# Kernel optimization log

Measured on AMD Instinct MI355X. Metric: run time of the kernel, lower is better.

Reference implementation:

```python
import jax, jax.numpy as jnp
import numpy as np
import math

NUM_HEADS = 16
NUM_KV_HEADS = 4
HEAD_DIM = 128
HIDDEN = 2048
ROPE_BASE = 10000.0


def setup_inputs() -> dict:
    key = jax.random.key(0)
    ks = jax.random.split(key, 6)
    B, S = 1, 4096
    hidden_states = jax.random.normal(ks[0], (B, S, HIDDEN), dtype=jnp.float32)
    attention_mask = jnp.ones((B, S), dtype=jnp.int32)
    position_ids = jnp.broadcast_to(jnp.arange(S, dtype=jnp.int32)[None, :], (B, S))
    sc = 1.0 / math.sqrt(HIDDEN)
    wq = jax.random.normal(ks[1], (HIDDEN, NUM_HEADS * HEAD_DIM), dtype=jnp.float32) * sc
    wk = jax.random.normal(ks[2], (HIDDEN, NUM_KV_HEADS * HEAD_DIM), dtype=jnp.float32) * sc
    wv = jax.random.normal(ks[3], (HIDDEN, NUM_KV_HEADS * HEAD_DIM), dtype=jnp.float32) * sc
    wo = jax.random.normal(ks[4], (NUM_HEADS * HEAD_DIM, HIDDEN), dtype=jnp.float32) * sc
    return {"hidden_states": hidden_states, "attention_mask": attention_mask,
            "position_ids": position_ids, "wq": wq, "wk": wk, "wv": wv, "wo": wo}


def _rotate_half(x):
    x1, x2 = jnp.split(x, 2, axis=-1)
    return jnp.concatenate((-x2, x1), axis=-1)


def _rope_tables(seq_len, dtype):
    inv_freq = 1.0 / (ROPE_BASE ** (jnp.arange(0, HEAD_DIM, 2, dtype=jnp.float32) / HEAD_DIM))
    t = jnp.arange(seq_len, dtype=jnp.float32)
    freqs = jnp.outer(t, inv_freq)                       # [S, hd/2]
    emb = jnp.concatenate((freqs, freqs), axis=-1)       # [S, hd]
    return jnp.cos(emb).astype(dtype), jnp.sin(emb).astype(dtype)


def reference(hidden_states, attention_mask, position_ids, wq, wk, wv, wo):
    B, S, _ = hidden_states.shape
    dtype = hidden_states.dtype
    # projections -> [B, H, S, hd]
    q = (hidden_states @ wq).reshape(B, S, NUM_HEADS, HEAD_DIM).transpose(0, 2, 1, 3)
    k = (hidden_states @ wk).reshape(B, S, NUM_KV_HEADS, HEAD_DIM).transpose(0, 2, 1, 3)
    v = (hidden_states @ wv).reshape(B, S, NUM_KV_HEADS, HEAD_DIM).transpose(0, 2, 1, 3)
    # RoPE
    cos_t, sin_t = _rope_tables(S, dtype)
    cos = cos_t[position_ids][:, None]                   # [B,1,S,hd]
    sin = sin_t[position_ids][:, None]
    q = q * cos + _rotate_half(q) * sin
    k = k * cos + _rotate_half(k) * sin
    # GQA repeat
    n_rep = NUM_HEADS // NUM_KV_HEADS
    k = jnp.repeat(k, n_rep, axis=1)
    v = jnp.repeat(v, n_rep, axis=1)
    # scores + causal mask + padding mask
    scores = jnp.einsum('bhqd,bhkd->bhqk', q, k) / math.sqrt(HEAD_DIM)
    neg = jnp.finfo(scores.dtype).min
    causal = jnp.triu(jnp.full((S, S), neg, dtype=scores.dtype), k=1)
    scores = scores + causal[None, None]
    pad = (1.0 - attention_mask.astype(scores.dtype))[:, None, None, :] * neg
    scores = scores + pad
    attn = jax.nn.softmax(scores.astype(jnp.float32), axis=-1).astype(dtype)
    out = jnp.einsum('bhqk,bhkd->bhqd', attn, v)
    out = out.transpose(0, 2, 1, 3).reshape(B, S, NUM_HEADS * HEAD_DIM)
    return out @ wo
```

## Files before the change

### kernel.cpp

```cpp
#include <hip/hip_runtime.h>
#include <cstdint>
#include <cstddef>

typedef unsigned short ushort_t;
typedef short    bf16x8 __attribute__((ext_vector_type(8)));
typedef float    f32x4  __attribute__((ext_vector_type(4)));
typedef uint4    __attribute__((may_alias)) uint4_a;
typedef ushort4  __attribute__((may_alias)) ushort4_a;
typedef float4   __attribute__((may_alias)) float4_a;
typedef float2   __attribute__((may_alias)) float2_a;
typedef unsigned __attribute__((may_alias)) uint_a;

constexpr int SEQ = 4096, HID = 2048, NHEADS = 16, NKVH = 4, HDIM = 128;
constexpr int QD  = NHEADS * HDIM;
constexpr int KVD = NKVH * HDIM;
constexpr int KVL = 2 * KVD;
constexpr int NPART = 56;

static __device__ __forceinline__ float bf2f(ushort_t u) {
    return __uint_as_float(((unsigned)u) << 16);
}
static __device__ __forceinline__ ushort_t f2bf(float f) {
    unsigned x = __float_as_uint(f);
    unsigned r = x + 0x7FFFu + ((x >> 16) & 1u);
    return (ushort_t)(r >> 16);
}
static __device__ __forceinline__ unsigned pack2(float lo, float hi) {
    return (unsigned)f2bf(lo) | ((unsigned)f2bf(hi) << 16);
}
static __device__ __forceinline__ unsigned cvt_pk(float lo, float hi) {
    unsigned r;
    asm("v_cvt_pk_bf16_f32 %0, %1, %2" : "=v"(r) : "v"(lo), "v"(hi));
    return r;
}

static __device__ __forceinline__ void gld16(const ushort_t* g, ushort_t* l) {
    __builtin_amdgcn_global_load_lds(
        (const __attribute__((address_space(1))) unsigned*)g,
        (__attribute__((address_space(3))) unsigned*)l, 16, 0, 0);
}

__global__ __launch_bounds__(256) void cast_f32_bf16(
    const float* __restrict__ in, ushort_t* __restrict__ out, int n)
{
    int i = (blockIdx.x * 256 + threadIdx.x) * 8;
    if (i >= n) return;
    float4 a = *(const float4_a*)(in + i);
    float4 b = *(const float4_a*)(in + i + 4);
    uint4 o;
    o.x = pack2(a.x, a.y); o.y = pack2(a.z, a.w);
    o.z = pack2(b.x, b.y); o.w = pack2(b.z, b.w);
    *(uint4_a*)(out + i) = o;
}

__global__ __launch_bounds__(256) void transpose_cast(
    const float* __restrict__ W, ushort_t* __restrict__ WT, int K, int N)
{
    __shared__ float tl[32][36];
    const int k0 = blockIdx.x * 32, n0 = blockIdx.y * 32;
    const int t  = threadIdx.x;
    {
        int i = t >> 3, jb = (t & 7) * 4;
        *(float4_a*)&tl[i][jb] = *(const float4_a*)(W + (size_t)(k0 + i) * N + n0 + jb);
    }
    __syncthreads();
    {
        int n = t >> 3, kb = (t & 7) * 4;
        ushort4 o;
        o.x = f2bf(tl[kb + 0][n]); o.y = f2bf(tl[kb + 1][n]);
        o.z = f2bf(tl[kb + 2][n]); o.w = f2bf(tl[kb + 3][n]);
        *(ushort4_a*)(WT + (size_t)(n0 + n) * K + k0 + kb) = o;
    }
}

__global__ __launch_bounds__(256) void gemm_mfma(
    const ushort_t* __restrict__ A, int lda,
    const ushort_t* __restrict__ Bt, int ldb,
    void* __restrict__ C1, int ld1, void* __restrict__ C2, int ld2,
    int split, int N, int K, int out_f32)
{
    __shared__ ushort_t as[128 * 32];
    __shared__ ushort_t bs[128 * 32];

    const int t    = threadIdx.x;
    const int mb   = blockIdx.y * 128, nb = blockIdx.x * 128;
    const int w    = t >> 6, lane = t & 63, quad = lane >> 4, l15 = lane & 15;
    const int wm   = (w >> 1) * 64, wn = (w & 1) * 64;

    const int dr_row = lane >> 2, dr_c = lane & 3;
    const int rA0 = w * 16 + dr_row, rA1 = 64 + w * 16 + dr_row;
    const ushort_t* a0p = A  + (size_t)(mb + rA0) * lda + (dr_c ^ (rA0 & 3)) * 8;
    const ushort_t* a1p = A  + (size_t)(mb + rA1) * lda + (dr_c ^ (rA1 & 3)) * 8;
    const ushort_t* b0p = Bt + (size_t)(nb + rA0) * ldb + (dr_c ^ (rA0 & 3)) * 8;
    const ushort_t* b1p = Bt + (size_t)(nb + rA1) * ldb + (dr_c ^ (rA1 & 3)) * 8;
    ushort_t* asb0 = &as[(w) * 512];        ushort_t* asb1 = &as[(4 + w) * 512];
    ushort_t* bsb0 = &bs[(w) * 512];        ushort_t* bsb1 = &bs[(4 + w) * 512];

    f32x4 acc[4][4];
#pragma unroll
    for (int i = 0; i < 4; i++)
#pragma unroll
        for (int j = 0; j < 4; j++) acc[i][j] = (f32x4)0.f;

    const int chunk = quad ^ (l15 & 3);

    for (int kb = 0; kb < K; kb += 32) {
        __syncthreads();
        gld16(a0p + kb, asb0);
        gld16(a1p + kb, asb1);
        gld16(b0p + kb, bsb0);
        gld16(b1p + kb, bsb1);
        __syncthreads();

        bf16x8 af[4], bf[4];
#pragma unroll
        for (int mt = 0; mt < 4; mt++)
            af[mt] = *(const bf16x8*)&as[(wm + mt * 16 + l15) * 32 + chunk * 8];
#pragma unroll
        for (int nt = 0; nt < 4; nt++)
            bf[nt] = *(const bf16x8*)&bs[(wn + nt * 16 + l15) * 32 + chunk * 8];
#pragma unroll
        for (int mt = 0; mt < 4; mt++)
#pragma unroll
            for (int nt = 0; nt < 4; nt++)
                acc[mt][nt] = __builtin_amdgcn_mfma_f32_16x16x32_bf16(
                    af[mt], bf[nt], acc[mt][nt], 0, 0, 0);
    }

#pragma unroll
    for (int mt = 0; mt < 4; mt++)
#pragma unroll
        for (int nt = 0; nt < 4; nt++) {
            int colg = nb + wn + nt * 16 + l15;
#pragma unroll
            for (int r = 0; r < 4; r++) {
                int row = mb + wm + mt * 16 + quad * 4 + r;
                float v = acc[mt][nt][r];
                if (out_f32)            ((float*)C1)[(size_t)row * ld1 + colg] = v;
                else if (colg < split)  ((ushort_t*)C1)[(size_t)row * ld1 + colg] = f2bf(v);
                else                    ((ushort_t*)C2)[(size_t)row * ld2 + colg - split] = f2bf(v);
            }
        }
}

__global__ __launch_bounds__(256) void rope_both(
    ushort_t* __restrict__ qb, ushort_t* __restrict__ kvb,
    const int* __restrict__ pos_ids)
{
    int idx  = blockIdx.x * 256 + threadIdx.x;
    int i    = idx & 63;
    int rem  = idx >> 6;
    int hs   = rem % (NHEADS + NKVH);
    int s    = rem / (NHEADS + NKVH);
    if (s >= SEQ) return;

    float pos = (float)pos_ids[s];
    float ang = pos * __expf(-(float)i * 0.14391156831212787f);
    float c, sn;
    sincosf(ang, &sn, &c);

    ushort_t* p = (hs < NHEADS)
        ? qb  + (size_t)s * QD  + hs * HDIM
        : kvb + (size_t)s * KVL + (hs - NHEADS) * HDIM;
    float x0 = bf2f(p[i]);
    float x1 = bf2f(p[i + 64]);
    p[i]      = f2bf(x0 * c - x1 * sn);
    p[i + 64] = f2bf(x1 * c + x0 * sn);
}

__global__ __launch_bounds__(512, 4) void flash_mfma(
    const ushort_t* Q, const ushort_t* __restrict__ KV,
    const int* __restrict__ amask, ushort_t* O,
    ushort_t* __restrict__ Opart, float2* __restrict__ ML)
{
    __shared__ ushort_t ks[64][136];
    __shared__ ushort_t vt[128][72];
    __shared__ float    bias[64];

    const int t = threadIdx.x, w = t >> 6, lane = t & 63;
    const int quad = lane >> 4, l15 = lane & 15;
    const int h = blockIdx.x, kvh = h >> 2;
    const int s = blockIdx.y;
    const int kcol = kvh * HDIM, vcol = KVD + kvh * HDIM;
    const float scale2 = 0.08838834764831845f * 1.44269504088896340f;

    int tile, ktb, kte, pid;
    bool multi;
    if (s < 8)       { tile = 15 - s;        ktb = 0; kte = 2 * tile + 2; multi = false; pid = 0; }
    else if (s < 64) {
        int cs = s - 8;
        int c;
        if (cs < 24) { tile = 16 + cs / 3; c = cs - (tile - 16) * 3; }
        else         { int d = cs - 24; tile = 24 + (d >> 2); c = d & 3; }
        int nkt = 2 * tile + 2;
        ktb = c * 16; kte = (ktb + 16 < nkt) ? ktb + 16 : nkt;
        multi = true; pid = h * NPART + cs;
    }
    else             { tile = 7 - (s - 64);  ktb = 0; kte = 2 * tile + 2; multi = false; pid = 0; }

    const int q0  = tile * 128;
    const int q0w = q0 + w * 16;

    const int krow = t >> 3,  kdo = (t & 7) * 16;
    const int vkp  = t & 31,  vdg = t >> 5;

    int bpi[4];
#pragma unroll
    for (int t4 = 0; t4 < 4; t4++)
        bpi[t4] = ((2 * (quad & 1) + (t4 >> 1)) * 16 + l15) * 4;
    const bool hi_half = (quad >> 1) != 0;

    bf16x8 qf[4];
    {
        const ushort_t* qp = Q + (size_t)(q0w + l15) * QD + h * HDIM;
#pragma unroll
        for (int c = 0; c < 4; c++)
            qf[c] = *(const bf16x8*)(qp + c * 32 + quad * 8);
    }

    f32x4 accO[8];
#pragma unroll
    for (int j = 0; j < 8; j++) accO[j] = (f32x4)0.f;
    float m_s = -1e30f, l_s = 0.f;

    uint4 kst[2], va, vb;
    float bst = 0.f;
    auto stage_load = [&](int kt) {
        const int k0 = kt * 64;
        const ushort_t* kp = KV + (size_t)(k0 + krow) * KVL + kcol + kdo;
        kst[0] = *(const uint4_a*)kp;
        kst[1] = *(const uint4_a*)(kp + 8);
        const ushort_t* vp = KV + (size_t)(k0 + 2 * vkp) * KVL + vcol + vdg * 8;
        va = *(const uint4_a*)vp;
        vb = *(const uint4_a*)(vp + KVL);
        if (t < 64) bst = amask[k0 + t] ? 0.f : -1e30f;
    };

    stage_load(ktb);

    for (int kt = ktb; kt < kte; kt++) {
        const int k0 = kt * 64;
        __syncthreads();
        *(uint4_a*)&ks[krow][kdo]     = kst[0];
        *(uint4_a*)&ks[krow][kdo + 8] = kst[1];
        {
            unsigned aw[4] = {va.x, va.y, va.z, va.w};
            unsigned bw[4] = {vb.x, vb.y, vb.z, vb.w};
#pragma unroll
            for (int i = 0; i < 4; i++) {
                *(uint_a*)&vt[vdg * 8 + 2 * i][2 * vkp] =
                    (aw[i] & 0xFFFFu) | (bw[i] << 16);
                *(uint_a*)&vt[vdg * 8 + 2 * i + 1][2 * vkp] =
                    (aw[i] >> 16) | (bw[i] & 0xFFFF0000u);
            }
        }
        if (t < 64) bias[t] = bst;
        __syncthreads();
        if (kt + 1 < kte) stage_load(kt + 1);

        if (k0 > q0w + 15) continue;

        f32x4 sx[4];
#pragma unroll
        for (int mt = 0; mt < 4; mt++) sx[mt] = (f32x4)0.f;
        __builtin_amdgcn_s_setprio(1);
#pragma unroll
        for (int c = 0; c < 4; c++)
#pragma unroll
            for (int mt = 0; mt < 4; mt++) {
                bf16x8 kf = *(const bf16x8*)&ks[mt * 16 + l15][c * 32 + quad * 8];
                sx[mt] = __builtin_amdgcn_mfma_f32_16x16x32_bf16(kf, qf[c], sx[mt], 0, 0, 0);
            }
        __builtin_amdgcn_s_setprio(0);

        const int qg = q0w + l15;
        const bool full = (k0 + 63 <= q0w);
        float p[4][4];
        float mx = -1e30f;
#pragma unroll
        for (int mt = 0; mt < 4; mt++) {
            float4 b4 = *(const float4_a*)&bias[mt * 16 + quad * 4];
            float br[4] = {b4.x, b4.y, b4.z, b4.w};
#pragma unroll
            for (int r = 0; r < 4; r++) {
                float v = fmaf(sx[mt][r], scale2, br[r]);
                if (!full) {
                    int kg = k0 + mt * 16 + quad * 4 + r;
                    v = (kg > qg) ? -1e30f : v;
                }
                p[mt][r] = v;
                mx = fmaxf(mx, v);
            }
        }
        mx = fmaxf(mx, __shfl_xor(mx, 16));
        mx = fmaxf(mx, __shfl_xor(mx, 32));
        const bool renorm = !__all(mx <= m_s + 8.f);
        const float mnew = renorm ? fmaxf(m_s, mx) : m_s;
        float sum = 0.f;
        unsigned wlo[4], whi[4];
#pragma unroll
        for (int mt = 0; mt < 4; mt++) {
            float p0 = exp2f(p[mt][0] - mnew);
            float p1 = exp2f(p[mt][1] - mnew);
            float p2 = exp2f(p[mt][2] - mnew);
            float p3 = exp2f(p[mt][3] - mnew);
            sum += (p0 + p1) + (p2 + p3);
            wlo[mt] = cvt_pk(p0, p1);
            whi[mt] = cvt_pk(p2, p3);
        }
        sum += __shfl_xor(sum, 16);
        sum += __shfl_xor(sum, 32);

        if (renorm) {
            float alpha = exp2f(m_s - mnew);
            l_s *= alpha;
            float a0 = __shfl(alpha, quad * 4 + 0);
            float a1 = __shfl(alpha, quad * 4 + 1);
            float a2 = __shfl(alpha, quad * 4 + 2);
            float a3 = __shfl(alpha, quad * 4 + 3);
#pragma unroll
            for (int j = 0; j < 8; j++) {
                f32x4 a = accO[j];
                a[0] *= a0; a[1] *= a1; a[2] *= a2; a[3] *= a3;
                accO[j] = a;
            }
        }
        m_s = mnew;
        l_s += sum;

#pragma unroll
        for (int kc = 0; kc < 2; kc++) {
            union { unsigned u[4]; bf16x8 v; } pf;
#pragma unroll
            for (int t4 = 0; t4 < 4; t4++) {
                unsigned slo = (t4 & 1) ? whi[2 * kc]     : wlo[2 * kc];
                unsigned shi = (t4 & 1) ? whi[2 * kc + 1] : wlo[2 * kc + 1];
                int ra = __builtin_amdgcn_ds_bpermute(bpi[t4], (int)slo);
                int rb = __builtin_amdgcn_ds_bpermute(bpi[t4], (int)shi);
                pf.u[t4] = (unsigned)(hi_half ? rb : ra);
            }
            __builtin_amdgcn_s_setprio(1);
#pragma unroll
            for (int n8 = 0; n8 < 8; n8++) {
                bf16x8 vf = *(const bf16x8*)&vt[n8 * 16 + l15][kc * 32 + quad * 8];
                accO[n8] = __builtin_amdgcn_mfma_f32_16x16x32_bf16(pf.v, vf, accO[n8], 0, 0, 0);
            }
            __builtin_amdgcn_s_setprio(0);
        }
    }

    if (!multi) {
        float linv = 1.0f / l_s;
#pragma unroll
        for (int r = 0; r < 4; r++) {
            float lr = __shfl(linv, quad * 4 + r);
            int row = q0w + quad * 4 + r;
            ushort_t* op = O + (size_t)row * QD + h * HDIM;
#pragma unroll
            for (int n8 = 0; n8 < 8; n8++)
                op[n8 * 16 + l15] = f2bf(accO[n8][r] * lr);
        }
    } else {
        ushort_t* op = Opart + (size_t)pid * (128 * 128);
#pragma unroll
        for (int r = 0; r < 4; r++) {
            int row = w * 16 + quad * 4 + r;
#pragma unroll
            for (int n8 = 0; n8 < 8; n8++)
                op[row * 128 + n8 * 16 + l15] = f2bf(accO[n8][r]);
        }
        if (quad == 0)
            ML[pid * 128 + w * 16 + l15] = make_float2(m_s, l_s);
    }
}

__global__ __launch_bounds__(256) void combine_partials(
    const ushort_t* __restrict__ P, const float2* __restrict__ ML,
    ushort_t* __restrict__ O)
{
    __shared__ float wc[4][128];
    const int h = blockIdx.x >> 4, tt = blockIdx.x & 15, tile = 16 + tt;
    const int nc = (tile < 24) ? 3 : 4;
    const int pid0 = h * NPART + ((tile < 24) ? tt * 3 : 24 + (tile - 24) * 4);
    const int tid = threadIdx.x;

    if (tid < 128) {
        const int row = tid;
        float m_[4], l_[4];
        float M = -1e30f;
#pragma unroll
        for (int c = 0; c < 4; c++) {
            if (c < nc) {
                float2 v = *(const float2_a*)&ML[(pid0 + c) * 128 + row];
                m_[c] = v.x; l_[c] = v.y; M = fmaxf(M, v.x);
            } else { m_[c] = -1e30f; l_[c] = 0.f; }
        }
        float L = 0.f, wgt[4];
#pragma unroll
        for (int c = 0; c < 4; c++) { wgt[c] = exp2f(m_[c] - M); L += wgt[c] * l_[c]; }
        const float inv = 1.0f / L;
#pragma unroll
        for (int c = 0; c < 4; c++) wc[c][row] = (c < nc) ? wgt[c] * inv : 0.f;
    }
    __syncthreads();

#pragma unroll
    for (int p = 0; p < 4; p++) {
        const int idx = p * 256 + tid;
        const int row = idx >> 3, seg = idx & 7;
        const size_t pb = (size_t)row * 128 + seg * 16;
        float acc[16];
#pragma unroll
        for (int j = 0; j < 16; j++) acc[j] = 0.f;
#pragma unroll
        for (int c = 0; c < 4; c++) {
            if (c < nc) {
                const ushort_t* pp = P + (size_t)(pid0 + c) * (128 * 128) + pb;
                uint4 v0 = *(const uint4_a*)pp;
                uint4 v1 = *(const uint4_a*)(pp + 8);
                const float wv_ = wc[c][row];
                unsigned u[8] = {v0.x, v0.y, v0.z, v0.w, v1.x, v1.y, v1.z, v1.w};
#pragma unroll
                for (int j = 0; j < 8; j++) {
                    acc[2 * j]     += wv_ * bf2f((ushort_t)(u[j] & 0xFFFFu));
                    acc[2 * j + 1] += wv_ * bf2f((ushort_t)(u[j] >> 16));
                }
            }
        }
        ushort_t* op = O + (size_t)(tile * 128 + row) * QD + h * HDIM + seg * 16;
        uint4 o0, o1;
        o0.x = pack2(acc[0],  acc[1]);  o0.y = pack2(acc[2],  acc[3]);
        o0.z = pack2(acc[4],  acc[5]);  o0.w = pack2(acc[6],  acc[7]);
        o1.x = pack2(acc[8],  acc[9]);  o1.y = pack2(acc[10], acc[11]);
        o1.z = pack2(acc[12], acc[13]); o1.w = pack2(acc[14], acc[15]);
        *(uint4_a*)op       = o0;
        *(uint4_a*)(op + 8) = o1;
    }
}

extern "C" void kernel_launch(void* const* d_in, const int* in_sizes, int n_in,
                              void* d_out, int out_size, void* d_ws, size_t ws_size,
                              hipStream_t stream)
{
    const float* x     = (const float*)d_in[0];
    const int*   amask = (const int*)d_in[1];
    const int*   pos   = (const int*)d_in[2];
    const float* wq    = (const float*)d_in[3];
    const float* wk    = (const float*)d_in[4];
    const float* wv    = (const float*)d_in[5];
    const float* wo    = (const float*)d_in[6];
    float* out = (float*)d_out;

    ushort_t* wqkvT = (ushort_t*)d_out;
    ushort_t* xb    = wqkvT + (size_t)3072 * HID;

    ushort_t* qbuf  = (ushort_t*)d_ws;
    ushort_t* kvbuf = qbuf + (size_t)SEQ * QD;
    ushort_t* woT   = kvbuf;

    ushort_t* opart = (ushort_t*)d_out;
    float2*   mlbuf = (float2*)((char*)d_out + (size_t)16 * NPART * 128 * 128 * 2);

    cast_f32_bf16<<<SEQ * HID / 8 / 256, 256, 0, stream>>>(x, xb, SEQ * HID);
    transpose_cast<<<dim3(HID / 32, QD / 32),  256, 0, stream>>>(wq, wqkvT, HID, QD);
    transpose_cast<<<dim3(HID / 32, KVD / 32), 256, 0, stream>>>(wk, wqkvT + (size_t)QD * HID, HID, KVD);
    transpose_cast<<<dim3(HID / 32, KVD / 32), 256, 0, stream>>>(wv, wqkvT + (size_t)(QD + KVD) * HID, HID, KVD);

    gemm_mfma<<<dim3(3072 / 128, SEQ / 128), 256, 0, stream>>>(
        xb, HID, wqkvT, HID, qbuf, QD, kvbuf, KVL, QD, 3072, HID, 0);

    rope_both<<<SEQ * (NHEADS + NKVH) * 64 / 256, 256, 0, stream>>>(qbuf, kvbuf, pos);

    flash_mfma<<<dim3(NHEADS, 72), 512, 0, stream>>>(
        qbuf, kvbuf, amask, qbuf, opart, mlbuf);
    combine_partials<<<dim3(256), 256, 0, stream>>>(opart, mlbuf, qbuf);

    transpose_cast<<<dim3(QD / 32, HID / 32), 256, 0, stream>>>(wo, woT, QD, HID);
    gemm_mfma<<<dim3(HID / 128, SEQ / 128), 256, 0, stream>>>(
        qbuf, QD, woT, QD, out, HID, out, HID, HID, HID, QD, 1);
}
```

Baseline: 449.2 us.

## Double-buffer flash attention K/V tiles with async LDS loads and swizzle

The flash attention kernel now keeps two LDS buffers for K, V^T and the mask bias. The next K tile is fetched with direct global-to-LDS loads (gld16) into an XOR-swizzled unpadded layout, and the next V tile is loaded into registers and stored after compute. This cuts the per-iteration barriers from two to one and overlaps loads with the MFMA work. The three QKV weight transpose launches are also merged into one kernel. The cost is doubled LDS use, which may limit occupancy under launch_bounds(512,4).

```diff
diff --git a/kernel.cpp b/kernel.cpp
--- a/kernel.cpp
+++ b/kernel.cpp
@@ -73,6 +73,31 @@
     }
 }
 
+__global__ __launch_bounds__(256) void transpose_cast_qkv(
+    const float* __restrict__ wq, const float* __restrict__ wk,
+    const float* __restrict__ wv, ushort_t* __restrict__ WT)
+{
+    __shared__ float tl[32][36];
+    const int k0 = blockIdx.x * 32, nb = blockIdx.y * 32;
+    const int t  = threadIdx.x;
+    const float* W; int n0, N;
+    if (nb < 2048)      { W = wq; n0 = nb;        N = QD;  }
+    else if (nb < 2560) { W = wk; n0 = nb - 2048; N = KVD; }
+    else                { W = wv; n0 = nb - 2560; N = KVD; }
+    {
+        int i = t >> 3, jb = (t & 7) * 4;
+        *(float4_a*)&tl[i][jb] = *(const float4_a*)(W + (size_t)(k0 + i) * N + n0 + jb);
+    }
+    __syncthreads();
+    {
+        int n = t >> 3, kb = (t & 7) * 4;
+        ushort4 o;
+        o.x = f2bf(tl[kb + 0][n]); o.y = f2bf(tl[kb + 1][n]);
+        o.z = f2bf(tl[kb + 2][n]); o.w = f2bf(tl[kb + 3][n]);
+        *(ushort4_a*)(WT + (size_t)(nb + n) * HID + k0 + kb) = o;
+    }
+}
+
 __global__ __launch_bounds__(256) void gemm_mfma(
     const ushort_t* __restrict__ A, int lda,
     const ushort_t* __restrict__ Bt, int ldb,
@@ -173,9 +198,9 @@
     const int* __restrict__ amask, ushort_t* O,
     ushort_t* __restrict__ Opart, float2* __restrict__ ML)
 {
-    __shared__ ushort_t ks[64][136];
-    __shared__ ushort_t vt[128][72];
-    __shared__ float    bias[64];
+    __shared__ ushort_t ks[2][64 * 128];
+    __shared__ ushort_t vt[2][128 * 72];
+    __shared__ float    bias[2][64];
 
     const int t = threadIdx.x, w = t >> 6, lane = t & 63;
     const int quad = lane >> 4, l15 = lane & 15;
@@ -201,7 +226,8 @@
     const int q0  = tile * 128;
     const int q0w = q0 + w * 16;
 
-    const int krow = t >> 3,  kdo = (t & 7) * 16;
+    const int kRow = w * 4 + quad;
+    const int klc  = l15 ^ (kRow & 7);
     const int vkp  = t & 31,  vdg = t >> 5;
 
     int bpi[4];
@@ -210,6 +236,11 @@
         bpi[t4] = ((2 * (quad & 1) + (t4 >> 1)) * 16 + l15) * 4;
     const bool hi_half = (quad >> 1) != 0;
 
+    int pco[4];
+#pragma unroll
+    for (int c = 0; c < 4; c++)
+        pco[c] = ((4 * c + quad) ^ (l15 & 7)) * 8;
+
     bf16x8 qf[4];
     {
         const ushort_t* qp = Q + (size_t)(q0w + l15) * QD + h * HDIM;
@@ -223,130 +254,138 @@
     for (int j = 0; j < 8; j++) accO[j] = (f32x4)0.f;
     float m_s = -1e30f, l_s = 0.f;
 
-    uint4 kst[2], va, vb;
+    uint4 va, vb;
     float bst = 0.f;
-    auto stage_load = [&](int kt) {
-        const int k0 = kt * 64;
-        const ushort_t* kp = KV + (size_t)(k0 + krow) * KVL + kcol + kdo;
-        kst[0] = *(const uint4_a*)kp;
-        kst[1] = *(const uint4_a*)(kp + 8);
-        const ushort_t* vp = KV + (size_t)(k0 + 2 * vkp) * KVL + vcol + vdg * 8;
+    auto stage_k = [&](int kt, int b) {
+        const ushort_t* g0 = KV + (size_t)(kt * 64 + kRow) * KVL + kcol + klc * 8;
+        gld16(g0, &ks[b][w * 512]);
+        gld16(g0 + (size_t)32 * KVL, &ks[b][4096 + w * 512]);
+    };
+    auto vload = [&](int kt) {
+        const ushort_t* vp = KV + (size_t)(kt * 64 + 2 * vkp) * KVL + vcol + vdg * 8;
         va = *(const uint4_a*)vp;
         vb = *(const uint4_a*)(vp + KVL);
-        if (t < 64) bst = amask[k0 + t] ? 0.f : -1e30f;
+        bst = (t < 64) ? (amask[kt * 64 + t] ? 0.f : -1e30f) : 0.f;
     };
-
-    stage_load(ktb);
+    auto vstore = [&](int b) {
+        unsigned aw[4] = {va.x, va.y, va.z, va.w};
+        unsigned bw[4] = {vb.x, vb.y, vb.z, vb.w};
+#pragma unroll
+        for (int i = 0; i < 4; i++) {
+            *(uint_a*)&vt[b][(vdg * 8 + 2 * i) * 72 + 2 * vkp] =
+                (aw[i] & 0xFFFFu) | (bw[i] << 16);
+            *(uint_a*)&vt[b][(vdg * 8 + 2 * i + 1) * 72 + 2 * vkp] =
+                (aw[i] >> 16) | (bw[i] & 0xFFFF0000u);
+        }
+        if (t < 64) bias[b][t] = bst;
+    };
+
+    stage_k(ktb, 0);
+    vload(ktb);
+    vstore(0);
+    __syncthreads();
 
     for (int kt = ktb; kt < kte; kt++) {
+        const int cur = (kt - ktb) & 1;
         const int k0 = kt * 64;
+        const bool more = (kt + 1 < kte);
+        if (more) {
+            stage_k(kt + 1, cur ^ 1);
+            vload(kt + 1);
+        }
+
+        if (k0 <= q0w + 15) {
+            f32x4 sx[4];
+#pragma unroll
+            for (int mt = 0; mt < 4; mt++) sx[mt] = (f32x4)0.f;
+            __builtin_amdgcn_s_setprio(1);
+#pragma unroll
+            for (int c = 0; c < 4; c++)
+#pragma unroll
+                for (int mt = 0; mt < 4; mt++) {
+                    bf16x8 kf = *(const bf16x8*)&ks[cur][(mt * 16 + l15) * 128 + pco[c]];
+                    sx[mt] = __builtin_amdgcn_mfma_f32_16x16x32_bf16(kf, qf[c], sx[mt], 0, 0, 0);
+                }
+            __builtin_amdgcn_s_setprio(0);
+
+            const int qg = q0w + l15;
+            const bool full = (k0 + 63 <= q0w);
+            float p[4][4];
+            float mx = -1e30f;
+#pragma unroll
+            for (int mt = 0; mt < 4; mt++) {
+                float4 b4 = *(const float4_a*)&bias[cur][mt * 16 + quad * 4];
+                float br[4] = {b4.x, b4.y, b4.z, b4.w};
+#pragma unroll
+                for (int r = 0; r < 4; r++) {
+                    float v = fmaf(sx[mt][r], scale2, br[r]);
+                    if (!full) {
+                        int kg = k0 + mt * 16 + quad * 4 + r;
+                        v = (kg > qg) ? -1e30f : v;
+                    }
+                    p[mt][r] = v;
+                    mx = fmaxf(mx, v);
+                }
+            }
+            mx = fmaxf(mx, __shfl_xor(mx, 16));
+            mx = fmaxf(mx, __shfl_xor(mx, 32));
+            const bool renorm = !__all(mx <= m_s + 8.f);
+            const float mnew = renorm ? fmaxf(m_s, mx) : m_s;
+            float sum = 0.f;
+            unsigned wlo[4], whi[4];
+#pragma unroll
+            for (int mt = 0; mt < 4; mt++) {
+                float p0 = exp2f(p[mt][0] - mnew);
+                float p1 = exp2f(p[mt][1] - mnew);
+                float p2 = exp2f(p[mt][2] - mnew);
+                float p3 = exp2f(p[mt][3] - mnew);
+                sum += (p0 + p1) + (p2 + p3);
+                wlo[mt] = cvt_pk(p0, p1);
+                whi[mt] = cvt_pk(p2, p3);
+            }
+            sum += __shfl_xor(sum, 16);
+            sum += __shfl_xor(sum, 32);
+
+            if (renorm) {
+                float alpha = exp2f(m_s - mnew);
+                l_s *= alpha;
+                float a0 = __shfl(alpha, quad * 4 + 0);
+                float a1 = __shfl(alpha, quad * 4 + 1);
+                float a2 = __shfl(alpha, quad * 4 + 2);
+                float a3 = __shfl(alpha, quad * 4 + 3);
+#pragma unroll
+                for (int j = 0; j < 8; j++) {
+                    f32x4 a = accO[j];
+                    a[0] *= a0; a[1] *= a1; a[2] *= a2; a[3] *= a3;
+                    accO[j] = a;
+                }
+            }
+            m_s = mnew;
+            l_s += sum;
+
+#pragma unroll
+            for (int kc = 0; kc < 2; kc++) {
+                union { unsigned u[4]; bf16x8 v; } pf;
+#pragma unroll
+                for (int t4 = 0; t4 < 4; t4++) {
+                    unsigned slo = (t4 & 1) ? whi[2 * kc]     : wlo[2 * kc];
+                    unsigned shi = (t4 & 1) ? whi[2 * kc + 1] : wlo[2 * kc + 1];
+                    int ra = __builtin_amdgcn_ds_bpermute(bpi[t4], (int)slo);
+                    int rb = __builtin_amdgcn_ds_bpermute(bpi[t4], (int)shi);
+                    pf.u[t4] = (unsigned)(hi_half ? rb : ra);
+                }
+                __builtin_amdgcn_s_setprio(1);
+#pragma unroll
+                for (int n8 = 0; n8 < 8; n8++) {
+                    bf16x8 vf = *(const bf16x8*)&vt[cur][(n8 * 16 + l15) * 72 + kc * 32 + quad * 8];
+                    accO[n8] = __builtin_amdgcn_mfma_f32_16x16x32_bf16(pf.v, vf, accO[n8], 0, 0, 0);
+                }
+                __builtin_amdgcn_s_setprio(0);
+            }
+        }
+
+        if (more) vstore(cur ^ 1);
         __syncthreads();
-        *(uint4_a*)&ks[krow][kdo]     = kst[0];
-        *(uint4_a*)&ks[krow][kdo + 8] = kst[1];
-        {
-            unsigned aw[4] = {va.x, va.y, va.z, va.w};
-            unsigned bw[4] = {vb.x, vb.y, vb.z, vb.w};
-#pragma unroll
-            for (int i = 0; i < 4; i++) {
-                *(uint_a*)&vt[vdg * 8 + 2 * i][2 * vkp] =
-                    (aw[i] & 0xFFFFu) | (bw[i] << 16);
-                *(uint_a*)&vt[vdg * 8 + 2 * i + 1][2 * vkp] =
-                    (aw[i] >> 16) | (bw[i] & 0xFFFF0000u);
-            }
-        }
-        if (t < 64) bias[t] = bst;
-        __syncthreads();
-        if (kt + 1 < kte) stage_load(kt + 1);
-
-        if (k0 > q0w + 15) continue;
-
-        f32x4 sx[4];
-#pragma unroll
-        for (int mt = 0; mt < 4; mt++) sx[mt] = (f32x4)0.f;
-        __builtin_amdgcn_s_setprio(1);
-#pragma unroll
-        for (int c = 0; c < 4; c++)
-#pragma unroll
-            for (int mt = 0; mt < 4; mt++) {
-                bf16x8 kf = *(const bf16x8*)&ks[mt * 16 + l15][c * 32 + quad * 8];
-                sx[mt] = __builtin_amdgcn_mfma_f32_16x16x32_bf16(kf, qf[c], sx[mt], 0, 0, 0);
-            }
-        __builtin_amdgcn_s_setprio(0);
-
-        const int qg = q0w + l15;
-        const bool full = (k0 + 63 <= q0w);
-        float p[4][4];
-        float mx = -1e30f;
-#pragma unroll
-        for (int mt = 0; mt < 4; mt++) {
-            float4 b4 = *(const float4_a*)&bias[mt * 16 + quad * 4];
-            float br[4] = {b4.x, b4.y, b4.z, b4.w};
-#pragma unroll
-            for (int r = 0; r < 4; r++) {
-                float v = fmaf(sx[mt][r], scale2, br[r]);
-                if (!full) {
-                    int kg = k0 + mt * 16 + quad * 4 + r;
-                    v = (kg > qg) ? -1e30f : v;
-                }
-                p[mt][r] = v;
-                mx = fmaxf(mx, v);
-            }
-        }
-        mx = fmaxf(mx, __shfl_xor(mx, 16));
-        mx = fmaxf(mx, __shfl_xor(mx, 32));
-        const bool renorm = !__all(mx <= m_s + 8.f);
-        const float mnew = renorm ? fmaxf(m_s, mx) : m_s;
-        float sum = 0.f;
-        unsigned wlo[4], whi[4];
-#pragma unroll
-        for (int mt = 0; mt < 4; mt++) {
-            float p0 = exp2f(p[mt][0] - mnew);
-            float p1 = exp2f(p[mt][1] - mnew);
-            float p2 = exp2f(p[mt][2] - mnew);
-            float p3 = exp2f(p[mt][3] - mnew);
-            sum += (p0 + p1) + (p2 + p3);
-            wlo[mt] = cvt_pk(p0, p1);
-            whi[mt] = cvt_pk(p2, p3);
-        }
-        sum += __shfl_xor(sum, 16);
-        sum += __shfl_xor(sum, 32);
-
-        if (renorm) {
-            float alpha = exp2f(m_s - mnew);
-            l_s *= alpha;
-            float a0 = __shfl(alpha, quad * 4 + 0);
-            float a1 = __shfl(alpha, quad * 4 + 1);
-            float a2 = __shfl(alpha, quad * 4 + 2);
-            float a3 = __shfl(alpha, quad * 4 + 3);
-#pragma unroll
-            for (int j = 0; j < 8; j++) {
-                f32x4 a = accO[j];
-                a[0] *= a0; a[1] *= a1; a[2] *= a2; a[3] *= a3;
-                accO[j] = a;
-            }
-        }
-        m_s = mnew;
-        l_s += sum;
-
-#pragma unroll
-        for (int kc = 0; kc < 2; kc++) {
-            union { unsigned u[4]; bf16x8 v; } pf;
-#pragma unroll
-            for (int t4 = 0; t4 < 4; t4++) {
-                unsigned slo = (t4 & 1) ? whi[2 * kc]     : wlo[2 * kc];
-                unsigned shi = (t4 & 1) ? whi[2 * kc + 1] : wlo[2 * kc + 1];
-                int ra = __builtin_amdgcn_ds_bpermute(bpi[t4], (int)slo);
-                int rb = __builtin_amdgcn_ds_bpermute(bpi[t4], (int)shi);
-                pf.u[t4] = (unsigned)(hi_half ? rb : ra);
-            }
-            __builtin_amdgcn_s_setprio(1);
-#pragma unroll
-            for (int n8 = 0; n8 < 8; n8++) {
-                bf16x8 vf = *(const bf16x8*)&vt[n8 * 16 + l15][kc * 32 + quad * 8];
-                accO[n8] = __builtin_amdgcn_mfma_f32_16x16x32_bf16(pf.v, vf, accO[n8], 0, 0, 0);
-            }
-            __builtin_amdgcn_s_setprio(0);
-        }
     }
 
     if (!multi) {
@@ -462,9 +501,7 @@
     float2*   mlbuf = (float2*)((char*)d_out + (size_t)16 * NPART * 128 * 128 * 2);
 
     cast_f32_bf16<<<SEQ * HID / 8 / 256, 256, 0, stream>>>(x, xb, SEQ * HID);
-    transpose_cast<<<dim3(HID / 32, QD / 32),  256, 0, stream>>>(wq, wqkvT, HID, QD);
-    transpose_cast<<<dim3(HID / 32, KVD / 32), 256, 0, stream>>>(wk, wqkvT + (size_t)QD * HID, HID, KVD);
-    transpose_cast<<<dim3(HID / 32, KVD / 32), 256, 0, stream>>>(wv, wqkvT + (size_t)(QD + KVD) * HID, HID, KVD);
+    transpose_cast_qkv<<<dim3(HID / 32, 3072 / 32), 256, 0, stream>>>(wq, wk, wv, wqkvT);
 
     gemm_mfma<<<dim3(3072 / 128, SEQ / 128), 256, 0, stream>>>(
         xb, HID, wqkvT, HID, qbuf, QD, kvbuf, KVL, QD, 3072, HID, 0);
```

Measured after the change: 424.6 us. -5.5%, faster.
